# Kernel optimization log

Hardware: AMD Instinct MI355X
Metric: run time of the kernel (lower is better)

The kernel has to match this reference:

```python
import jax, jax.numpy as jnp
import numpy as np

B, N, K = 256, 1024, 64          # batch, atoms per structure, abc combinations
E = 2 * K                        # embedding_dim = 128
NSG = 230                        # number of space groups
LN_EPS = 1e-5


def setup_inputs() -> dict:
    key = jax.random.key(0)
    ks = jax.random.split(key, 12)
    xav = float(np.sqrt(6.0 / (K + K)))  # xavier_uniform bound for [K,K] slices
    return {
        "atom_positions": jax.random.uniform(ks[0], (B, N, 3), dtype=jnp.float32),
        "reciprocal_matrices": jax.random.normal(ks[1], (B, 3, 3), dtype=jnp.float32),
        "space_group": jax.random.randint(ks[2], (B, 1), 1, NSG + 1, dtype=jnp.int32),
        "abc_combinations": jax.random.normal(ks[3], (K, 3), dtype=jnp.float32),
        "graphs_array": jax.random.uniform(ks[4], (NSG, K, K), dtype=jnp.float32),
        "w_real": jax.random.uniform(ks[5], (NSG, K, K), jnp.float32, -xav, xav),
        "w_imag": jax.random.uniform(ks[6], (NSG, K, K), jnp.float32, -xav, xav),
        "b_real": jnp.zeros((NSG, K), jnp.float32),
        "b_imag": jnp.zeros((NSG, K), jnp.float32),
        "W2": jax.random.normal(ks[7], (E, E), dtype=jnp.float32) * 0.05,
        "b2": jnp.zeros((E,), jnp.float32),
        "gamma": jnp.ones((E,), jnp.float32),
        "beta": jnp.zeros((E,), jnp.float32),
    }


def reference(atom_positions, reciprocal_matrices, space_group, abc_combinations,
              graphs_array, w_real, w_imag, b_real, b_imag, W2, b2, gamma, beta):
    sg = space_group[:, 0] - 1                                  # [B] in [0,229]
    # transformed_abc = abc @ recip^T : [B,K,3]
    t_abc = jnp.einsum('kc,bdc->bkd', abc_combinations, reciprocal_matrices)
    # encodings = exp(i*2pi * pos @ t_abc^T) : [B,N,K] complex
    phase = (2.0 * jnp.pi) * jnp.einsum('bnc,bkc->bnk', atom_positions, t_abc)
    enc = jax.lax.complex(jnp.cos(phase), jnp.sin(phase))
    # per-sample adjacency gather + complex batched matmul
    adj = graphs_array[sg]                                      # [B,K,K]
    weighted = jnp.einsum('bnk,bkm->bnm', enc, adj.astype(enc.dtype))
    weighted = weighted[:, :, :K]                               # slice to embedding_dim//2
    # SpaceGroupDenseLayer: per-sample complex expert weights
    Wc = jax.lax.complex(w_real, w_imag)[sg]                    # [B,K,K]
    bc = jax.lax.complex(b_real, b_imag)[sg][:, None, :]        # [B,1,K]
    out_c = jnp.einsum('bni,bif->bnf', weighted, Wc) + bc       # [B,N,K] complex
    x = jnp.concatenate([out_c.real, out_c.imag], axis=-1)      # [B,N,2K]
    x = jax.nn.silu(x)
    x = x @ W2.T + b2                                           # Linear(E,E)
    mu = jnp.mean(x, axis=-1, keepdims=True)
    var = jnp.mean(jnp.square(x - mu), axis=-1, keepdims=True)
    return (x - mu) * jax.lax.rsqrt(var + LN_EPS) * gamma + beta
```

## Files before the change

kernel.cpp:

```cpp
#include <hip/hip_runtime.h>
#include <math.h>

#define BB 256
#define NN 1024
#define KK 64
#define EE 128
#define TM 64

typedef _Float16 half8 __attribute__((ext_vector_type(8)));
typedef float f32x4 __attribute__((ext_vector_type(4)));

__device__ __forceinline__ int swz(int row, int halfcol) {
    return (row * EE + halfcol) ^ ((row & 7) << 3);
}

__device__ __forceinline__ void gload_lds16(const void* g, void* l) {
    __builtin_amdgcn_global_load_lds(
        (const __attribute__((address_space(1))) unsigned int*)g,
        (__attribute__((address_space(3))) unsigned int*)l, 16, 0, 0);
}

__global__ __launch_bounds__(256) void prep_kernel(
    const float* __restrict__ recip,
    const int* __restrict__ space_group,
    const float* __restrict__ graphs,
    const float* __restrict__ w_real,
    const float* __restrict__ w_imag,
    const float* __restrict__ b_real,
    const float* __restrict__ b_imag,
    const float* __restrict__ W2,
    _Float16* __restrict__ Mt,
    float* __restrict__ bbout,
    _Float16* __restrict__ W2h)
{
    const int b = blockIdx.x;
    const int t = threadIdx.x;
    const int sg = space_group[b] - 1;

    if (b < EE * EE / 256) {
        const int idx = b * 256 + t;
        W2h[idx] = (_Float16)W2[idx];
    }

    __shared__ float adjL[KK * KK];
    __shared__ float wrL[KK * KK];
    __shared__ float wiL[KK * KK];

    const float* adjG = graphs + (size_t)sg * KK * KK;
    const float* wrG  = w_real + (size_t)sg * KK * KK;
    const float* wiG  = w_imag + (size_t)sg * KK * KK;
    for (int idx = t; idx < KK * KK; idx += 256) {
        adjL[idx] = adjG[idx];
        wrL[idx]  = wrG[idx];
        wiL[idx]  = wiG[idx];
    }
    __syncthreads();

    const int i  = t >> 2;
    const int f0 = (t & 3) * 16;
    float cr[16], ci[16];
#pragma unroll
    for (int c = 0; c < 16; ++c) { cr[c] = 0.f; ci[c] = 0.f; }
    for (int k = 0; k < KK; ++k) {
        const float a = adjL[i * KK + k];
#pragma unroll
        for (int c = 0; c < 16; ++c) {
            cr[c] += a * wrL[k * KK + f0 + c];
            ci[c] += a * wiL[k * KK + f0 + c];
        }
    }
    _Float16* Mb = Mt + (size_t)b * EE * EE;
#pragma unroll
    for (int c = 0; c < 16; ++c) {
        const int f = f0 + c;
        Mb[f * EE + i]             = (_Float16)cr[c];
        Mb[f * EE + KK + i]        = (_Float16)(-ci[c]);
        Mb[(KK + f) * EE + i]      = (_Float16)ci[c];
        Mb[(KK + f) * EE + KK + i] = (_Float16)cr[c];
    }
    if (t < EE) {
        bbout[b * EE + t] = (t < KK) ? b_real[sg * KK + t] : b_imag[sg * KK + (t - KK)];
    }
}

__global__ __launch_bounds__(256) void main_kernel(
    const float* __restrict__ pos,
    const float* __restrict__ recip,
    const float* __restrict__ abc,
    const _Float16* __restrict__ Mt,
    const float* __restrict__ bball,
    const _Float16* __restrict__ W2h,
    const float* __restrict__ b2,
    const float* __restrict__ gamma,
    const float* __restrict__ beta,
    float* __restrict__ out)
{
    const int d = blockIdx.x;
    const int j  = d >> 3;
    const int b  = (d & 7) * 32 + (j >> 4);
    const int n0 = (j & 15) * TM;
    const int t  = threadIdx.x;
    const int w    = t >> 6;
    const int lane = t & 63;
    const int ln15 = lane & 15;
    const int kg   = lane >> 4;

    __shared__ __align__(16) _Float16 Bt[EE * EE];
    __shared__ __align__(16) _Float16 X[TM * EE];
    __shared__ float abcL[KK * 3];

    if (t < KK * 3) abcL[t] = abc[t];
    __syncthreads();

    {
        const char* src = (const char*)(Mt + (size_t)b * EE * EE);
#pragma unroll
        for (int i = 0; i < 8; ++i) {
            const int c16 = t + i * 256;
            const int row = c16 >> 4;
            const int sl  = c16 & 15;
            const int g   = row * 16 + (sl ^ (row & 7));
            gload_lds16(src + g * 16, (char*)Bt + c16 * 16);
        }
    }

    const int grow = n0 + w * 16 + ln15;
    const float* pr = pos + ((size_t)b * NN + grow) * 3;
    const float px = pr[0], py = pr[1], pz = pr[2];
    const float* R = recip + b * 9;
    const float u0 = px * R[0] + py * R[3] + pz * R[6];
    const float u1 = px * R[1] + py * R[4] + pz * R[7];
    const float u2 = px * R[2] + py * R[5] + pz * R[8];

    half8 afrag[4];
#pragma unroll
    for (int mq = 0; mq < 2; ++mq) {
        _Float16 cb[8], sb[8];
#pragma unroll
        for (int jj = 0; jj < 8; ++jj) {
            const int k = mq * 32 + kg * 8 + jj;
            const float ph = 6.28318530717958647692f *
                (u0 * abcL[k * 3 + 0] + u1 * abcL[k * 3 + 1] + u2 * abcL[k * 3 + 2]);
            float s, c;
            __sincosf(ph, &s, &c);
            cb[jj] = (_Float16)c;
            sb[jj] = (_Float16)s;
        }
        afrag[mq]     = *(half8*)cb;
        afrag[mq + 2] = *(half8*)sb;
    }
    __syncthreads();

    f32x4 acc[8];
#pragma unroll
    for (int nt = 0; nt < 8; ++nt) {
        const int n = nt * 16 + ln15;
        f32x4 a = {0.f, 0.f, 0.f, 0.f};
#pragma unroll
        for (int kc = 0; kc < 4; ++kc) {
            const half8 bf = *(const half8*)&Bt[swz(n, kc * 32 + kg * 8)];
            a = __builtin_amdgcn_mfma_f32_16x16x32_f16(afrag[kc], bf, a, 0, 0, 0);
        }
        acc[nt] = a;
    }

#pragma unroll
    for (int nt = 0; nt < 8; ++nt) {
        const int col = nt * 16 + ln15;
        const float bbv = bball[b * EE + col];
#pragma unroll
        for (int r2 = 0; r2 < 4; ++r2) {
            const float v = acc[nt][r2] + bbv;
            const int rr = w * 16 + kg * 4 + r2;
            X[swz(rr, col)] = (_Float16)(v / (1.f + __expf(-v)));
        }
    }
    __syncthreads();

    {
        const char* src = (const char*)W2h;
#pragma unroll
        for (int i = 0; i < 8; ++i) {
            const int c16 = t + i * 256;
            const int row = c16 >> 4;
            const int sl  = c16 & 15;
            const int g   = row * 16 + (sl ^ (row & 7));
            gload_lds16(src + g * 16, (char*)Bt + c16 * 16);
        }
    }

    const int arow = w * 16 + ln15;
    half8 a2[4];
#pragma unroll
    for (int kc = 0; kc < 4; ++kc)
        a2[kc] = *(const half8*)&X[swz(arow, kc * 32 + kg * 8)];
    __syncthreads();

    f32x4 acc2[8];
#pragma unroll
    for (int nt = 0; nt < 8; ++nt) {
        const int n = nt * 16 + ln15;
        f32x4 a = {0.f, 0.f, 0.f, 0.f};
#pragma unroll
        for (int kc = 0; kc < 4; ++kc) {
            const half8 bf = *(const half8*)&Bt[swz(n, kc * 32 + kg * 8)];
            a = __builtin_amdgcn_mfma_f32_16x16x32_f16(a2[kc], bf, a, 0, 0, 0);
        }
        acc2[nt] = a;
    }

    float y[8][4];
    float s[4] = {0.f, 0.f, 0.f, 0.f}, q[4] = {0.f, 0.f, 0.f, 0.f};
#pragma unroll
    for (int nt = 0; nt < 8; ++nt) {
        const int col = nt * 16 + ln15;
        const float b2v = b2[col];
#pragma unroll
        for (int r2 = 0; r2 < 4; ++r2) {
            const float v = acc2[nt][r2] + b2v;
            y[nt][r2] = v;
            s[r2] += v;
            q[r2] += v * v;
        }
    }
#pragma unroll
    for (int m = 1; m < 16; m <<= 1) {
#pragma unroll
        for (int r2 = 0; r2 < 4; ++r2) {
            s[r2] += __shfl_xor(s[r2], m);
            q[r2] += __shfl_xor(q[r2], m);
        }
    }
    const float inv = 1.f / EE;
    float mu[4], rs[4];
#pragma unroll
    for (int r2 = 0; r2 < 4; ++r2) {
        mu[r2] = s[r2] * inv;
        rs[r2] = rsqrtf(fmaxf(q[r2] * inv - mu[r2] * mu[r2], 0.f) + 1e-5f);
    }
#pragma unroll
    for (int nt = 0; nt < 8; ++nt) {
        const int col = nt * 16 + ln15;
        const float g  = gamma[col];
        const float be = beta[col];
#pragma unroll
        for (int r2 = 0; r2 < 4; ++r2) {
            const int rr = w * 16 + kg * 4 + r2;
            out[((size_t)b * NN + n0 + rr) * EE + col] = (y[nt][r2] - mu[r2]) * rs[r2] * g + be;
        }
    }
}

extern "C" void kernel_launch(void* const* d_in, const int* in_sizes, int n_in,
                              void* d_out, int out_size, void* d_ws, size_t ws_size,
                              hipStream_t stream) {
    const float* pos    = (const float*)d_in[0];
    const float* recip  = (const float*)d_in[1];
    const int*   sgp    = (const int*)d_in[2];
    const float* abc    = (const float*)d_in[3];
    const float* graphs = (const float*)d_in[4];
    const float* wr     = (const float*)d_in[5];
    const float* wi     = (const float*)d_in[6];
    const float* br     = (const float*)d_in[7];
    const float* bi     = (const float*)d_in[8];
    const float* W2     = (const float*)d_in[9];
    const float* b2     = (const float*)d_in[10];
    const float* gm     = (const float*)d_in[11];
    const float* bt     = (const float*)d_in[12];
    float* out = (float*)d_out;

    char* ws = (char*)d_ws;
    _Float16* Mt    = (_Float16*)ws;
    _Float16* W2h   = (_Float16*)(ws + (size_t)BB * EE * EE * 2);
    float*    bball = (float*)(ws + (size_t)BB * EE * EE * 2 + 32768);

    hipLaunchKernelGGL(prep_kernel, dim3(BB), dim3(256), 0, stream,
                       recip, sgp, graphs, wr, wi, br, bi, W2, Mt, bball, W2h);
    hipLaunchKernelGGL(main_kernel, dim3(BB * NN / TM), dim3(256), 0, stream,
                       pos, recip, abc, Mt, bball, W2h, b2, gm, bt, out);
}
```

Measured before the change: 70.21 us.

## Split waves into 2x2 grid to reuse LDS B fragments across row tiles

Reorganizes the four waves from 16-row full-width strips into a 2x2 grid where each wave computes 32 rows by 64 columns, so each B fragment loaded from LDS feeds two MFMAs. This halves LDS reads of the weight tiles in both GEMMs. In exchange each wave computes sincos encodings for 32 rows (duplicating transcendental work across column waves), and LayerNorm statistics now need a cross-wave reduction through shared memory with an extra barrier.

Measured after the change: 77.94 us. 1.11x slower.

```diff
diff --git a/kernel.cpp b/kernel.cpp
--- a/kernel.cpp
+++ b/kernel.cpp
@@ -101,6 +101,8 @@
     const int n0 = (j & 15) * TM;
     const int t  = threadIdx.x;
     const int w    = t >> 6;
+    const int wr   = w >> 1;
+    const int wc   = w & 1;
     const int lane = t & 63;
     const int ln15 = lane & 15;
     const int kg   = lane >> 4;
@@ -108,6 +110,7 @@
     __shared__ __align__(16) _Float16 Bt[EE * EE];
     __shared__ __align__(16) _Float16 X[TM * EE];
     __shared__ float abcL[KK * 3];
+    __shared__ float2 pbuf[TM][2];
 
     if (t < KK * 3) abcL[t] = abc[t];
     __syncthreads();
@@ -124,55 +127,64 @@
         }
     }
 
-    const int grow = n0 + w * 16 + ln15;
-    const float* pr = pos + ((size_t)b * NN + grow) * 3;
-    const float px = pr[0], py = pr[1], pz = pr[2];
-    const float* R = recip + b * 9;
-    const float u0 = px * R[0] + py * R[3] + pz * R[6];
-    const float u1 = px * R[1] + py * R[4] + pz * R[7];
-    const float u2 = px * R[2] + py * R[5] + pz * R[8];
-
-    half8 afrag[4];
-#pragma unroll
-    for (int mq = 0; mq < 2; ++mq) {
-        _Float16 cb[8], sb[8];
-#pragma unroll
-        for (int jj = 0; jj < 8; ++jj) {
-            const int k = mq * 32 + kg * 8 + jj;
-            const float ph = 6.28318530717958647692f *
-                (u0 * abcL[k * 3 + 0] + u1 * abcL[k * 3 + 1] + u2 * abcL[k * 3 + 2]);
-            float s, c;
-            __sincosf(ph, &s, &c);
-            cb[jj] = (_Float16)c;
-            sb[jj] = (_Float16)s;
-        }
-        afrag[mq]     = *(half8*)cb;
-        afrag[mq + 2] = *(half8*)sb;
-    }
-    __syncthreads();
-
-    f32x4 acc[8];
-#pragma unroll
-    for (int nt = 0; nt < 8; ++nt) {
-        const int n = nt * 16 + ln15;
-        f32x4 a = {0.f, 0.f, 0.f, 0.f};
+    half8 afrag[2][4];
+#pragma unroll
+    for (int rt = 0; rt < 2; ++rt) {
+        const int grow = n0 + wr * 32 + rt * 16 + ln15;
+        const float* pr = pos + ((size_t)b * NN + grow) * 3;
+        const float px = pr[0], py = pr[1], pz = pr[2];
+        const float* R = recip + b * 9;
+        const float u0 = px * R[0] + py * R[3] + pz * R[6];
+        const float u1 = px * R[1] + py * R[4] + pz * R[7];
+        const float u2 = px * R[2] + py * R[5] + pz * R[8];
+#pragma unroll
+        for (int mq = 0; mq < 2; ++mq) {
+            _Float16 cb[8], sb[8];
+#pragma unroll
+            for (int jj = 0; jj < 8; ++jj) {
+                const int k = mq * 32 + kg * 8 + jj;
+                const float ph = 6.28318530717958647692f *
+                    (u0 * abcL[k * 3 + 0] + u1 * abcL[k * 3 + 1] + u2 * abcL[k * 3 + 2]);
+                float s, c;
+                __sincosf(ph, &s, &c);
+                cb[jj] = (_Float16)c;
+                sb[jj] = (_Float16)s;
+            }
+            afrag[rt][mq]     = *(half8*)cb;
+            afrag[rt][mq + 2] = *(half8*)sb;
+        }
+    }
+    __syncthreads();
+
+    f32x4 acc[2][4];
+#pragma unroll
+    for (int rt = 0; rt < 2; ++rt)
+#pragma unroll
+        for (int ct = 0; ct < 4; ++ct) acc[rt][ct] = (f32x4){0.f, 0.f, 0.f, 0.f};
+
+#pragma unroll
+    for (int ct = 0; ct < 4; ++ct) {
+        const int n = wc * 64 + ct * 16 + ln15;
 #pragma unroll
         for (int kc = 0; kc < 4; ++kc) {
             const half8 bf = *(const half8*)&Bt[swz(n, kc * 32 + kg * 8)];
-            a = __builtin_amdgcn_mfma_f32_16x16x32_f16(afrag[kc], bf, a, 0, 0, 0);
-        }
-        acc[nt] = a;
-    }
-
-#pragma unroll
-    for (int nt = 0; nt < 8; ++nt) {
-        const int col = nt * 16 + ln15;
+            acc[0][ct] = __builtin_amdgcn_mfma_f32_16x16x32_f16(afrag[0][kc], bf, acc[0][ct], 0, 0, 0);
+            acc[1][ct] = __builtin_amdgcn_mfma_f32_16x16x32_f16(afrag[1][kc], bf, acc[1][ct], 0, 0, 0);
+        }
+    }
+
+#pragma unroll
+    for (int ct = 0; ct < 4; ++ct) {
+        const int col = wc * 64 + ct * 16 + ln15;
         const float bbv = bball[b * EE + col];
 #pragma unroll
-        for (int r2 = 0; r2 < 4; ++r2) {
-            const float v = acc[nt][r2] + bbv;
-            const int rr = w * 16 + kg * 4 + r2;
-            X[swz(rr, col)] = (_Float16)(v / (1.f + __expf(-v)));
+        for (int rt = 0; rt < 2; ++rt) {
+#pragma unroll
+            for (int r2 = 0; r2 < 4; ++r2) {
+                const float v = acc[rt][ct][r2] + bbv;
+                const int rr = wr * 32 + rt * 16 + kg * 4 + r2;
+                X[swz(rr, col)] = (_Float16)(v / (1.f + __expf(-v)));
+            }
         }
     }
     __syncthreads();
@@ -189,64 +201,99 @@
         }
     }
 
-    const int arow = w * 16 + ln15;
-    half8 a2[4];
-#pragma unroll
-    for (int kc = 0; kc < 4; ++kc)
-        a2[kc] = *(const half8*)&X[swz(arow, kc * 32 + kg * 8)];
-    __syncthreads();
-
-    f32x4 acc2[8];
-#pragma unroll
-    for (int nt = 0; nt < 8; ++nt) {
-        const int n = nt * 16 + ln15;
-        f32x4 a = {0.f, 0.f, 0.f, 0.f};
+    half8 a2[2][4];
+#pragma unroll
+    for (int rt = 0; rt < 2; ++rt)
+#pragma unroll
+        for (int kc = 0; kc < 4; ++kc)
+            a2[rt][kc] = *(const half8*)&X[swz(wr * 32 + rt * 16 + ln15, kc * 32 + kg * 8)];
+    __syncthreads();
+
+    f32x4 acc2[2][4];
+#pragma unroll
+    for (int rt = 0; rt < 2; ++rt)
+#pragma unroll
+        for (int ct = 0; ct < 4; ++ct) acc2[rt][ct] = (f32x4){0.f, 0.f, 0.f, 0.f};
+
+#pragma unroll
+    for (int ct = 0; ct < 4; ++ct) {
+        const int n = wc * 64 + ct * 16 + ln15;
 #pragma unroll
         for (int kc = 0; kc < 4; ++kc) {
             const half8 bf = *(const half8*)&Bt[swz(n, kc * 32 + kg * 8)];
-            a = __builtin_amdgcn_mfma_f32_16x16x32_f16(a2[kc], bf, a, 0, 0, 0);
-        }
-        acc2[nt] = a;
-    }
-
-    float y[8][4];
-    float s[4] = {0.f, 0.f, 0.f, 0.f}, q[4] = {0.f, 0.f, 0.f, 0.f};
-#pragma unroll
-    for (int nt = 0; nt < 8; ++nt) {
-        const int col = nt * 16 + ln15;
+            acc2[0][ct] = __builtin_amdgcn_mfma_f32_16x16x32_f16(a2[0][kc], bf, acc2[0][ct], 0, 0, 0);
+            acc2[1][ct] = __builtin_amdgcn_mfma_f32_16x16x32_f16(a2[1][kc], bf, acc2[1][ct], 0, 0, 0);
+        }
+    }
+
+#pragma unroll
+    for (int ct = 0; ct < 4; ++ct) {
+        const int col = wc * 64 + ct * 16 + ln15;
         const float b2v = b2[col];
 #pragma unroll
+        for (int rt = 0; rt < 2; ++rt)
+#pragma unroll
+            for (int r2 = 0; r2 < 4; ++r2) acc2[rt][ct][r2] += b2v;
+    }
+    float ps[2][4], pq[2][4];
+#pragma unroll
+    for (int rt = 0; rt < 2; ++rt) {
+#pragma unroll
         for (int r2 = 0; r2 < 4; ++r2) {
-            const float v = acc2[nt][r2] + b2v;
-            y[nt][r2] = v;
-            s[r2] += v;
-            q[r2] += v * v;
-        }
-    }
-#pragma unroll
-    for (int m = 1; m < 16; m <<= 1) {
+            float s = 0.f, q = 0.f;
+#pragma unroll
+            for (int ct = 0; ct < 4; ++ct) {
+                const float v = acc2[rt][ct][r2];
+                s += v; q += v * v;
+            }
+#pragma unroll
+            for (int m = 1; m < 16; m <<= 1) {
+                s += __shfl_xor(s, m);
+                q += __shfl_xor(q, m);
+            }
+            ps[rt][r2] = s; pq[rt][r2] = q;
+        }
+    }
+    if (ln15 == 0) {
+#pragma unroll
+        for (int rt = 0; rt < 2; ++rt)
+#pragma unroll
+            for (int r2 = 0; r2 < 4; ++r2) {
+                const int rr = wr * 32 + rt * 16 + kg * 4 + r2;
+                pbuf[rr][wc] = make_float2(ps[rt][r2], pq[rt][r2]);
+            }
+    }
+    __syncthreads();
+
+    const float inv = 1.f / EE;
+    float mu[2][4], rs[2][4];
+#pragma unroll
+    for (int rt = 0; rt < 2; ++rt) {
 #pragma unroll
         for (int r2 = 0; r2 < 4; ++r2) {
-            s[r2] += __shfl_xor(s[r2], m);
-            q[r2] += __shfl_xor(q[r2], m);
-        }
-    }
-    const float inv = 1.f / EE;
-    float mu[4], rs[4];
-#pragma unroll
-    for (int r2 = 0; r2 < 4; ++r2) {
-        mu[r2] = s[r2] * inv;
-        rs[r2] = rsqrtf(fmaxf(q[r2] * inv - mu[r2] * mu[r2], 0.f) + 1e-5f);
-    }
-#pragma unroll
-    for (int nt = 0; nt < 8; ++nt) {
-        const int col = nt * 16 + ln15;
+            const int rr = wr * 32 + rt * 16 + kg * 4 + r2;
+            const float2 pa = pbuf[rr][0];
+            const float2 pb = pbuf[rr][1];
+            const float s = pa.x + pb.x;
+            const float q = pa.y + pb.y;
+            const float m = s * inv;
+            mu[rt][r2] = m;
+            rs[rt][r2] = rsqrtf(fmaxf(q * inv - m * m, 0.f) + 1e-5f);
+        }
+    }
+#pragma unroll
+    for (int ct = 0; ct < 4; ++ct) {
+        const int col = wc * 64 + ct * 16 + ln15;
         const float g  = gamma[col];
         const float be = beta[col];
 #pragma unroll
-        for (int r2 = 0; r2 < 4; ++r2) {
-            const int rr = w * 16 + kg * 4 + r2;
-            out[((size_t)b * NN + n0 + rr) * EE + col] = (y[nt][r2] - mu[r2]) * rs[r2] * g + be;
+        for (int rt = 0; rt < 2; ++rt) {
+#pragma unroll
+            for (int r2 = 0; r2 < 4; ++r2) {
+                const int rr = wr * 32 + rt * 16 + kg * 4 + r2;
+                out[((size_t)b * NN + n0 + rr) * EE + col] =
+                    (acc2[rt][ct][r2] - mu[rt][r2]) * rs[rt][r2] * g + be;
+            }
         }
     }
 }
```

## Make main kernel persistent over row tiles, loading M and W2 into LDS once

Applied to the files above, without the earlier changes.

The main kernel now launches 512 blocks, each looping over 8 row tiles of one batch sample. Both the per-sample M matrix and W2 stay resident in separate LDS buffers, so the repeated global-to-LDS loads and the associated barriers are removed. The transformed abc vectors are precomputed per sample in the prep kernel, and the bias, gamma and beta values are hoisted into registers. In exchange, LDS use grows to about 80 KB per block, which lowers occupancy, and the grid gives less parallelism with no overlap between tiles inside a block.

After: 97.23 us. 1.38x slower.

```diff
diff --git a/kernel.cpp b/kernel.cpp
--- a/kernel.cpp
+++ b/kernel.cpp
@@ -6,6 +6,7 @@
 #define KK 64
 #define EE 128
 #define TM 64
+#define NT 8
 
 typedef _Float16 half8 __attribute__((ext_vector_type(8)));
 typedef float f32x4 __attribute__((ext_vector_type(4)));
@@ -23,6 +24,7 @@
 __global__ __launch_bounds__(256) void prep_kernel(
     const float* __restrict__ recip,
     const int* __restrict__ space_group,
+    const float* __restrict__ abc,
     const float* __restrict__ graphs,
     const float* __restrict__ w_real,
     const float* __restrict__ w_imag,
@@ -31,6 +33,7 @@
     const float* __restrict__ W2,
     _Float16* __restrict__ Mt,
     float* __restrict__ bbout,
+    float* __restrict__ tabcP,
     _Float16* __restrict__ W2h)
 {
     const int b = blockIdx.x;
@@ -81,14 +84,23 @@
     if (t < EE) {
         bbout[b * EE + t] = (t < KK) ? b_real[sg * KK + t] : b_imag[sg * KK + (t - KK)];
     }
+    if (t < KK) {
+        const float a0 = abc[t * 3 + 0], a1 = abc[t * 3 + 1], a2 = abc[t * 3 + 2];
+        const float* R = recip + b * 9;
+        float4 v;
+        v.x = a0 * R[0] + a1 * R[1] + a2 * R[2];
+        v.y = a0 * R[3] + a1 * R[4] + a2 * R[5];
+        v.z = a0 * R[6] + a1 * R[7] + a2 * R[8];
+        v.w = 0.f;
+        *(float4*)&tabcP[((size_t)b * KK + t) * 4] = v;
+    }
 }
 
 __global__ __launch_bounds__(256) void main_kernel(
     const float* __restrict__ pos,
-    const float* __restrict__ recip,
-    const float* __restrict__ abc,
     const _Float16* __restrict__ Mt,
     const float* __restrict__ bball,
+    const float* __restrict__ tabcP,
     const _Float16* __restrict__ W2h,
     const float* __restrict__ b2,
     const float* __restrict__ gamma,
@@ -96,157 +108,151 @@
     float* __restrict__ out)
 {
     const int d = blockIdx.x;
-    const int j  = d >> 3;
-    const int b  = (d & 7) * 32 + (j >> 4);
-    const int n0 = (j & 15) * TM;
+    const int idx = d >> 3;
+    const int b    = (d & 7) * 32 + (idx >> 1);
+    const int half = idx & 1;
     const int t  = threadIdx.x;
     const int w    = t >> 6;
     const int lane = t & 63;
     const int ln15 = lane & 15;
     const int kg   = lane >> 4;
 
-    __shared__ __align__(16) _Float16 Bt[EE * EE];
+    __shared__ __align__(16) _Float16 BtM[EE * EE];
+    __shared__ __align__(16) _Float16 BtW[EE * EE];
     __shared__ __align__(16) _Float16 X[TM * EE];
-    __shared__ float abcL[KK * 3];
-
-    if (t < KK * 3) abcL[t] = abc[t];
-    __syncthreads();
 
     {
-        const char* src = (const char*)(Mt + (size_t)b * EE * EE);
+        const char* srcM = (const char*)(Mt + (size_t)b * EE * EE);
+        const char* srcW = (const char*)W2h;
 #pragma unroll
         for (int i = 0; i < 8; ++i) {
             const int c16 = t + i * 256;
             const int row = c16 >> 4;
             const int sl  = c16 & 15;
             const int g   = row * 16 + (sl ^ (row & 7));
-            gload_lds16(src + g * 16, (char*)Bt + c16 * 16);
-        }
-    }
-
-    const int grow = n0 + w * 16 + ln15;
-    const float* pr = pos + ((size_t)b * NN + grow) * 3;
-    const float px = pr[0], py = pr[1], pz = pr[2];
-    const float* R = recip + b * 9;
-    const float u0 = px * R[0] + py * R[3] + pz * R[6];
-    const float u1 = px * R[1] + py * R[4] + pz * R[7];
-    const float u2 = px * R[2] + py * R[5] + pz * R[8];
-
-    half8 afrag[4];
-#pragma unroll
-    for (int mq = 0; mq < 2; ++mq) {
-        _Float16 cb[8], sb[8];
-#pragma unroll
-        for (int jj = 0; jj < 8; ++jj) {
-            const int k = mq * 32 + kg * 8 + jj;
-            const float ph = 6.28318530717958647692f *
-                (u0 * abcL[k * 3 + 0] + u1 * abcL[k * 3 + 1] + u2 * abcL[k * 3 + 2]);
-            float s, c;
-            __sincosf(ph, &s, &c);
-            cb[jj] = (_Float16)c;
-            sb[jj] = (_Float16)s;
-        }
-        afrag[mq]     = *(half8*)cb;
-        afrag[mq + 2] = *(half8*)sb;
-    }
-    __syncthreads();
-
-    f32x4 acc[8];
-#pragma unroll
-    for (int nt = 0; nt < 8; ++nt) {
-        const int n = nt * 16 + ln15;
-        f32x4 a = {0.f, 0.f, 0.f, 0.f};
-#pragma unroll
-        for (int kc = 0; kc < 4; ++kc) {
-            const half8 bf = *(const half8*)&Bt[swz(n, kc * 32 + kg * 8)];
-            a = __builtin_amdgcn_mfma_f32_16x16x32_f16(afrag[kc], bf, a, 0, 0, 0);
-        }
-        acc[nt] = a;
-    }
-
+            gload_lds16(srcM + g * 16, (char*)BtM + c16 * 16);
+            gload_lds16(srcW + g * 16, (char*)BtW + c16 * 16);
+        }
+    }
+
+    float bbv[8], b2v[8], gv[8], bev[8];
 #pragma unroll
     for (int nt = 0; nt < 8; ++nt) {
         const int col = nt * 16 + ln15;
-        const float bbv = bball[b * EE + col];
+        bbv[nt] = bball[b * EE + col];
+        b2v[nt] = b2[col];
+        gv[nt]  = gamma[col];
+        bev[nt] = beta[col];
+    }
+    const float* tp = tabcP + (size_t)b * KK * 4;
+
+    for (int tt = 0; tt < NT; ++tt) {
+        const int n0 = (half * NT + tt) * TM;
+
+        const int grow = n0 + w * 16 + ln15;
+        const float* pr = pos + ((size_t)b * NN + grow) * 3;
+        const float px = pr[0], py = pr[1], pz = pr[2];
+
+        half8 afrag[4];
+#pragma unroll
+        for (int mq = 0; mq < 2; ++mq) {
+            _Float16 cb[8], sb[8];
+#pragma unroll
+            for (int jj = 0; jj < 8; ++jj) {
+                const int k = mq * 32 + kg * 8 + jj;
+                const float4 tv = *(const float4*)&tp[k * 4];
+                const float ph = 6.28318530717958647692f *
+                    (px * tv.x + py * tv.y + pz * tv.z);
+                float s, c;
+                __sincosf(ph, &s, &c);
+                cb[jj] = (_Float16)c;
+                sb[jj] = (_Float16)s;
+            }
+            afrag[mq]     = *(half8*)cb;
+            afrag[mq + 2] = *(half8*)sb;
+        }
+
+        __syncthreads();
+
+        f32x4 acc[8];
+#pragma unroll
+        for (int nt = 0; nt < 8; ++nt) {
+            const int n = nt * 16 + ln15;
+            f32x4 a = {0.f, 0.f, 0.f, 0.f};
+#pragma unroll
+            for (int kc = 0; kc < 4; ++kc) {
+                const half8 bf = *(const half8*)&BtM[swz(n, kc * 32 + kg * 8)];
+                a = __builtin_amdgcn_mfma_f32_16x16x32_f16(afrag[kc], bf, a, 0, 0, 0);
+            }
+            acc[nt] = a;
+        }
+
+#pragma unroll
+        for (int nt = 0; nt < 8; ++nt) {
+            const int col = nt * 16 + ln15;
+#pragma unroll
+            for (int r2 = 0; r2 < 4; ++r2) {
+                const float v = acc[nt][r2] + bbv[nt];
+                const int rr = w * 16 + kg * 4 + r2;
+                X[swz(rr, col)] = (_Float16)(v / (1.f + __expf(-v)));
+            }
+        }
+        __syncthreads();
+
+        const int arow = w * 16 + ln15;
+        half8 a2[4];
+#pragma unroll
+        for (int kc = 0; kc < 4; ++kc)
+            a2[kc] = *(const half8*)&X[swz(arow, kc * 32 + kg * 8)];
+
+        f32x4 acc2[8];
+#pragma unroll
+        for (int nt = 0; nt < 8; ++nt) {
+            const int n = nt * 16 + ln15;
+            f32x4 a = {0.f, 0.f, 0.f, 0.f};
+#pragma unroll
+            for (int kc = 0; kc < 4; ++kc) {
+                const half8 bf = *(const half8*)&BtW[swz(n, kc * 32 + kg * 8)];
+                a = __builtin_amdgcn_mfma_f32_16x16x32_f16(a2[kc], bf, a, 0, 0, 0);
+            }
+            acc2[nt] = a;
+        }
+
+        float s[4] = {0.f, 0.f, 0.f, 0.f}, q[4] = {0.f, 0.f, 0.f, 0.f};
+#pragma unroll
+        for (int nt = 0; nt < 8; ++nt) {
+#pragma unroll
+            for (int r2 = 0; r2 < 4; ++r2) {
+                const float v = acc2[nt][r2] + b2v[nt];
+                acc2[nt][r2] = v;
+                s[r2] += v;
+                q[r2] += v * v;
+            }
+        }
+#pragma unroll
+        for (int m = 1; m < 16; m <<= 1) {
+#pragma unroll
+            for (int r2 = 0; r2 < 4; ++r2) {
+                s[r2] += __shfl_xor(s[r2], m);
+                q[r2] += __shfl_xor(q[r2], m);
+            }
+        }
+        const float inv = 1.f / EE;
+        float mu[4], rs[4];
 #pragma unroll
         for (int r2 = 0; r2 < 4; ++r2) {
-            const float v = acc[nt][r2] + bbv;
-            const int rr = w * 16 + kg * 4 + r2;
-            X[swz(rr, col)] = (_Float16)(v / (1.f + __expf(-v)));
-        }
-    }
-    __syncthreads();
-
-    {
-        const char* src = (const char*)W2h;
-#pragma unroll
-        for (int i = 0; i < 8; ++i) {
-            const int c16 = t + i * 256;
-            const int row = c16 >> 4;
-            const int sl  = c16 & 15;
-            const int g   = row * 16 + (sl ^ (row & 7));
-            gload_lds16(src + g * 16, (char*)Bt + c16 * 16);
-        }
-    }
-
-    const int arow = w * 16 + ln15;
-    half8 a2[4];
-#pragma unroll
-    for (int kc = 0; kc < 4; ++kc)
-        a2[kc] = *(const half8*)&X[swz(arow, kc * 32 + kg * 8)];
-    __syncthreads();
-
-    f32x4 acc2[8];
-#pragma unroll
-    for (int nt = 0; nt < 8; ++nt) {
-        const int n = nt * 16 + ln15;
-        f32x4 a = {0.f, 0.f, 0.f, 0.f};
-#pragma unroll
-        for (int kc = 0; kc < 4; ++kc) {
-            const half8 bf = *(const half8*)&Bt[swz(n, kc * 32 + kg * 8)];
-            a = __builtin_amdgcn_mfma_f32_16x16x32_f16(a2[kc], bf, a, 0, 0, 0);
-        }
-        acc2[nt] = a;
-    }
-
-    float y[8][4];
-    float s[4] = {0.f, 0.f, 0.f, 0.f}, q[4] = {0.f, 0.f, 0.f, 0.f};
-#pragma unroll
-    for (int nt = 0; nt < 8; ++nt) {
-        const int col = nt * 16 + ln15;
-        const float b2v = b2[col];
-#pragma unroll
-        for (int r2 = 0; r2 < 4; ++r2) {
-            const float v = acc2[nt][r2] + b2v;
-            y[nt][r2] = v;
-            s[r2] += v;
-            q[r2] += v * v;
-        }
-    }
-#pragma unroll
-    for (int m = 1; m < 16; m <<= 1) {
-#pragma unroll
-        for (int r2 = 0; r2 < 4; ++r2) {
-            s[r2] += __shfl_xor(s[r2], m);
-            q[r2] += __shfl_xor(q[r2], m);
-        }
-    }
-    const float inv = 1.f / EE;
-    float mu[4], rs[4];
-#pragma unroll
-    for (int r2 = 0; r2 < 4; ++r2) {
-        mu[r2] = s[r2] * inv;
-        rs[r2] = rsqrtf(fmaxf(q[r2] * inv - mu[r2] * mu[r2], 0.f) + 1e-5f);
-    }
-#pragma unroll
-    for (int nt = 0; nt < 8; ++nt) {
-        const int col = nt * 16 + ln15;
-        const float g  = gamma[col];
-        const float be = beta[col];
-#pragma unroll
-        for (int r2 = 0; r2 < 4; ++r2) {
-            const int rr = w * 16 + kg * 4 + r2;
-            out[((size_t)b * NN + n0 + rr) * EE + col] = (y[nt][r2] - mu[r2]) * rs[r2] * g + be;
+            mu[r2] = s[r2] * inv;
+            rs[r2] = rsqrtf(fmaxf(q[r2] * inv - mu[r2] * mu[r2], 0.f) + 1e-5f);
+        }
+#pragma unroll
+        for (int nt = 0; nt < 8; ++nt) {
+            const int col = nt * 16 + ln15;
+#pragma unroll
+            for (int r2 = 0; r2 < 4; ++r2) {
+                const int rr = w * 16 + kg * 4 + r2;
+                out[((size_t)b * NN + n0 + rr) * EE + col] =
+                    (acc2[nt][r2] - mu[r2]) * rs[r2] * gv[nt] + bev[nt];
+            }
         }
     }
 }
@@ -271,11 +277,13 @@
 
     char* ws = (char*)d_ws;
     _Float16* Mt    = (_Float16*)ws;
-    _Float16* W2h   = (_Float16*)(ws + (size_t)BB * EE * EE * 2);
-    float*    bball = (float*)(ws + (size_t)BB * EE * EE * 2 + 32768);
+    char* p = ws + (size_t)BB * EE * EE * 2;
+    _Float16* W2h   = (_Float16*)p;            p += EE * EE * 2;
+    float*    bball = (float*)p;               p += (size_t)BB * EE * 4;
+    float*    tabcP = (float*)p;
 
     hipLaunchKernelGGL(prep_kernel, dim3(BB), dim3(256), 0, stream,
-                       recip, sgp, graphs, wr, wi, br, bi, W2, Mt, bball, W2h);
-    hipLaunchKernelGGL(main_kernel, dim3(BB * NN / TM), dim3(256), 0, stream,
-                       pos, recip, abc, Mt, bball, W2h, b2, gm, bt, out);
-}
+                       recip, sgp, abc, graphs, wr, wi, br, bi, W2, Mt, bball, tabcP, W2h);
+    hipLaunchKernelGGL(main_kernel, dim3(512), dim3(256), 0, stream,
+                       pos, Mt, bball, tabcP, W2h, b2, gm, bt, out);
+}
```
